# Performance work log

Measured on AMD Instinct MI355X. Metric: run time of the kernel, lower is better.

Reference implementation:

```python
import jax, jax.numpy as jnp
import numpy as np

N_NODES = 50000


def gcn_layer(x, src, dst, W, b):
    # GCNConv: out = D^{-1/2} (A + I) D^{-1/2} (x W) + b
    n = x.shape[0]
    h = x @ W  # [N, C_out]
    # degree including self-loop (count of incoming edges at dst + 1)
    deg = jnp.zeros((n,), dtype=x.dtype).at[dst].add(1.0) + 1.0
    dinv_sqrt = jax.lax.rsqrt(deg)
    norm = dinv_sqrt[src] * dinv_sqrt[dst]  # [E]
    agg = jax.ops.segment_sum(h[src] * norm[:, None], dst, num_segments=n)
    # self-loop contribution: norm_ii = 1/deg_i
    agg = agg + h * (dinv_sqrt * dinv_sqrt)[:, None]
    return agg + b


def setup_inputs() -> dict:
    key = jax.random.key(0)
    k1, k2, k3, k4, k5, k6 = jax.random.split(key, 6)
    in_c, hid_c, out_c = 128, 128, 64
    x = jax.random.normal(k1, (N_NODES, in_c), dtype=jnp.float32)
    edge_index = jax.random.randint(k2, (2, 600000), 0, N_NODES, dtype=jnp.int64)
    W1 = jax.random.normal(k3, (in_c, hid_c), dtype=jnp.float32) * (1.0 / np.sqrt(in_c))
    b1 = jnp.zeros((hid_c,), dtype=jnp.float32)
    W2 = jax.random.normal(k4, (hid_c, out_c), dtype=jnp.float32) * (1.0 / np.sqrt(hid_c))
    b2 = jnp.zeros((out_c,), dtype=jnp.float32)
    return {"x": x, "edge_index": edge_index, "W1": W1, "b1": b1, "W2": W2, "b2": b2}


def reference(x, edge_index, W1, b1, W2, b2):
    src, dst = edge_index[0], edge_index[1]
    h = gcn_layer(x, src, dst, W1, b1)
    h = jax.nn.relu(h)
    out = gcn_layer(h, src, dst, W2, b2)
    return out
```

## Files before the change

kernel.cpp:

```cpp
#include <hip/hip_runtime.h>

#define IN_C 128
#define HID_C 128
#define OUT_C 64
#define CAP 40

typedef unsigned int uint;
typedef unsigned short ushort;
typedef __attribute__((ext_vector_type(8))) short short8;
typedef __attribute__((ext_vector_type(4))) float f32x4;

__device__ __forceinline__ float bf2f(ushort u) {
    return __uint_as_float(((uint)u) << 16);
}
__device__ __forceinline__ ushort f2bf(float f) {
    uint u = __float_as_uint(f);
    return (ushort)((u + 0x7fffu + ((u >> 16) & 1u)) >> 16);
}


__global__ void prep0_kernel(int* __restrict__ cursor, int n,
                             const float* __restrict__ W1, ushort* __restrict__ w1h,
                             ushort* __restrict__ w1l, const float* __restrict__ W2,
                             ushort* __restrict__ w2h, ushort* __restrict__ w2l) {
    int idx = blockIdx.x * blockDim.x + threadIdx.x;
    if (idx < n) {
        cursor[idx] = 0;
    } else if (idx < n + 128 * 128) {
        int i1 = idx - n;
        int k = i1 >> 7, c = i1 & 127;
        float w = W1[i1];
        ushort h = f2bf(w);
        ushort l = f2bf(w - bf2f(h));
        w1h[c * 128 + k] = h;
        w1l[c * 128 + k] = l;
    } else if (idx < n + 128 * 128 + 128 * 64) {
        int i2 = idx - n - 128 * 128;
        int k = i2 >> 6, c = i2 & 63;
        float w = W2[i2];
        ushort h = f2bf(w);
        ushort l = f2bf(w - bf2f(h));
        w2h[c * 128 + k] = h;
        w2l[c * 128 + k] = l;
    }
}


#define LSTR 40

__global__ __launch_bounds__(256) void gemm1_edge_kernel(
    const float* __restrict__ A, const ushort* __restrict__ BTh,
    const ushort* __restrict__ BTl, ushort* __restrict__ C, int M, int gblocks,
    const int* __restrict__ src, const int* __restrict__ dst,
    int* __restrict__ cursor, int* __restrict__ csr_src, int E) {
    constexpr int BN = 128;
    constexpr int NT = BN / 16;
    __shared__ ushort sAh[64 * LSTR], sAl[64 * LSTR];
    __shared__ ushort sBh[BN * LSTR], sBl[BN * LSTR];

    const int tid = threadIdx.x;

    if (blockIdx.x >= gblocks) {
        int e = (blockIdx.x - gblocks) * 256 + tid;
        if (e < E) {
            unsigned s = (unsigned)src[e];
            unsigned d = (unsigned)dst[e];
            if (s < (unsigned)M && d < (unsigned)M) {
                int p = atomicAdd(&cursor[d], 1);
                if (p < CAP) csr_src[d * CAP + p] = (int)s;
            }
        }
        return;
    }

    const int w = tid >> 6;
    const int lane = tid & 63;
    const int m = lane & 15;
    const int quad = lane >> 4;
    const int r0 = blockIdx.x * 64;

    f32x4 acc[NT];
#pragma unroll
    for (int t = 0; t < NT; ++t) acc[t] = (f32x4){0.f, 0.f, 0.f, 0.f};

    for (int k0 = 0; k0 < 128; k0 += 32) {
#pragma unroll
        for (int it = 0; it < 2; ++it) {
            int idx = tid + it * 256;
            int row = idx >> 3;
            int c4 = idx & 7;
            int grow = r0 + row;
            float4 v = make_float4(0.f, 0.f, 0.f, 0.f);
            if (grow < M) v = *(const float4*)&A[(size_t)grow * 128 + k0 + c4 * 4];
            ushort h0 = f2bf(v.x), h1 = f2bf(v.y), h2 = f2bf(v.z), h3 = f2bf(v.w);
            ushort l0 = f2bf(v.x - bf2f(h0)), l1 = f2bf(v.y - bf2f(h1));
            ushort l2 = f2bf(v.z - bf2f(h2)), l3 = f2bf(v.w - bf2f(h3));
            *(ushort4*)&sAh[row * LSTR + c4 * 4] = make_ushort4(h0, h1, h2, h3);
            *(ushort4*)&sAl[row * LSTR + c4 * 4] = make_ushort4(l0, l1, l2, l3);
        }
        for (int idx = tid; idx < BN * 4; idx += 256) {
            int row = idx >> 2;
            int c = idx & 3;
            *(uint4*)&sBh[row * LSTR + c * 8] = *(const uint4*)&BTh[row * 128 + k0 + c * 8];
            *(uint4*)&sBl[row * LSTR + c * 8] = *(const uint4*)&BTl[row * 128 + k0 + c * 8];
        }
        __syncthreads();

        short8 ah = *(const short8*)&sAh[(w * 16 + m) * LSTR + quad * 8];
        short8 al = *(const short8*)&sAl[(w * 16 + m) * LSTR + quad * 8];
#pragma unroll
        for (int t = 0; t < NT; ++t) {
            short8 bh = *(const short8*)&sBh[(t * 16 + m) * LSTR + quad * 8];
            short8 bl = *(const short8*)&sBl[(t * 16 + m) * LSTR + quad * 8];
            acc[t] = __builtin_amdgcn_mfma_f32_16x16x32_bf16(ah, bh, acc[t], 0, 0, 0);
            acc[t] = __builtin_amdgcn_mfma_f32_16x16x32_bf16(al, bh, acc[t], 0, 0, 0);
            acc[t] = __builtin_amdgcn_mfma_f32_16x16x32_bf16(ah, bl, acc[t], 0, 0, 0);
        }
        __syncthreads();
    }

#pragma unroll
    for (int t = 0; t < NT; ++t) {
#pragma unroll
        for (int r = 0; r < 4; ++r) {
            int row = r0 + w * 16 + quad * 4 + r;
            if (row < M) C[(size_t)row * BN + t * 16 + m] = f2bf(acc[t][r]);
        }
    }
}


template <int BN>
__global__ __launch_bounds__(256) void gemm_mfma_bf16A(const ushort* __restrict__ A,
                                                       const ushort* __restrict__ BTh,
                                                       const ushort* __restrict__ BTl,
                                                       ushort* __restrict__ C, int M) {
    constexpr int NT = BN / 16;
    __shared__ ushort sA[64 * LSTR];
    __shared__ ushort sBh[BN * LSTR], sBl[BN * LSTR];

    const int tid = threadIdx.x;
    const int w = tid >> 6;
    const int lane = tid & 63;
    const int m = lane & 15;
    const int quad = lane >> 4;
    const int r0 = blockIdx.x * 64;

    f32x4 acc[NT];
#pragma unroll
    for (int t = 0; t < NT; ++t) acc[t] = (f32x4){0.f, 0.f, 0.f, 0.f};

    for (int k0 = 0; k0 < 128; k0 += 32) {
        {
            int row = tid >> 2;
            int c = tid & 3;
            int grow = r0 + row;
            uint4 v = make_uint4(0, 0, 0, 0);
            if (grow < M) v = *(const uint4*)&A[(size_t)grow * 128 + k0 + c * 8];
            *(uint4*)&sA[row * LSTR + c * 8] = v;
        }
        for (int idx = tid; idx < BN * 4; idx += 256) {
            int row = idx >> 2;
            int c = idx & 3;
            *(uint4*)&sBh[row * LSTR + c * 8] = *(const uint4*)&BTh[row * 128 + k0 + c * 8];
            *(uint4*)&sBl[row * LSTR + c * 8] = *(const uint4*)&BTl[row * 128 + k0 + c * 8];
        }
        __syncthreads();

        short8 ah = *(const short8*)&sA[(w * 16 + m) * LSTR + quad * 8];
#pragma unroll
        for (int t = 0; t < NT; ++t) {
            short8 bh = *(const short8*)&sBh[(t * 16 + m) * LSTR + quad * 8];
            short8 bl = *(const short8*)&sBl[(t * 16 + m) * LSTR + quad * 8];
            acc[t] = __builtin_amdgcn_mfma_f32_16x16x32_bf16(ah, bh, acc[t], 0, 0, 0);
            acc[t] = __builtin_amdgcn_mfma_f32_16x16x32_bf16(ah, bl, acc[t], 0, 0, 0);
        }
        __syncthreads();
    }

#pragma unroll
    for (int t = 0; t < NT; ++t) {
#pragma unroll
        for (int r = 0; r < 4; ++r) {
            int row = r0 + w * 16 + quad * 4 + r;
            if (row < M) C[(size_t)row * BN + t * 16 + m] = f2bf(acc[t][r]);
        }
    }
}


__global__ __launch_bounds__(256) void agg128_kernel(
    const ushort4* __restrict__ h4, const int* __restrict__ csr_src,
    const int* __restrict__ degs, const float* __restrict__ bias,
    ushort4* __restrict__ out, int n) {
    int node = blockIdx.x * 4 + (threadIdx.x >> 6);
    if (node >= n) return;
    int lane = threadIdx.x & 63;
    int half = lane >> 5;
    int q = lane & 31;
    int cnt = min(degs[node], CAP);
    float degf = (float)(cnt + 1);
    float dinv_d = rsqrtf(degf);
    int start = node * CAP;
    float a0 = 0.f, a1 = 0.f, a2 = 0.f, a3 = 0.f;

    {
        int rem = cnt;
        int es = (lane < rem) ? csr_src[start + lane] : 0;
        int cs = (lane < rem) ? degs[es] : 0;
        float en = rsqrtf((float)(cs + 1)) * dinv_d;
        int j = 0;
#define A128_PAIR(J)                                                     \
        {                                                                \
            int s0 = __shfl(es, (J)), s1 = __shfl(es, (J) + 1);          \
            float n0 = __shfl(en, (J)), n1 = __shfl(en, (J) + 1);        \
            int ss = half ? s1 : s0;                                     \
            float nn = half ? n1 : n0;                                   \
            ushort4 v = h4[(size_t)ss * 32 + q];                         \
            a0 += nn * bf2f(v.x); a1 += nn * bf2f(v.y);                  \
            a2 += nn * bf2f(v.z); a3 += nn * bf2f(v.w);                  \
        }
        for (; j + 8 <= rem; j += 8) {
            A128_PAIR(j); A128_PAIR(j + 2); A128_PAIR(j + 4); A128_PAIR(j + 6);
        }
        for (; j + 2 <= rem; j += 2) { A128_PAIR(j); }
        if (j < rem) {
            int s0 = __shfl(es, j);
            float n0 = __shfl(en, j);
            float nn = half ? 0.f : n0;
            ushort4 v = h4[(size_t)s0 * 32 + q];
            a0 += nn * bf2f(v.x); a1 += nn * bf2f(v.y);
            a2 += nn * bf2f(v.z); a3 += nn * bf2f(v.w);
        }
#undef A128_PAIR
    }

    a0 += __shfl_xor(a0, 32);
    a1 += __shfl_xor(a1, 32);
    a2 += __shfl_xor(a2, 32);
    a3 += __shfl_xor(a3, 32);
    if (half == 0) {
        ushort4 sv = h4[(size_t)node * 32 + q];
        float sn = 1.0f / degf;
        float4 bq = ((const float4*)bias)[q];
        a0 = fmaxf(a0 + bf2f(sv.x) * sn + bq.x, 0.f);
        a1 = fmaxf(a1 + bf2f(sv.y) * sn + bq.y, 0.f);
        a2 = fmaxf(a2 + bf2f(sv.z) * sn + bq.z, 0.f);
        a3 = fmaxf(a3 + bf2f(sv.w) * sn + bq.w, 0.f);
        out[(size_t)node * 32 + q] = make_ushort4(f2bf(a0), f2bf(a1), f2bf(a2), f2bf(a3));
    }
}


__global__ __launch_bounds__(256) void agg64_kernel(
    const ushort4* __restrict__ h4, const int* __restrict__ csr_src,
    const int* __restrict__ degs, const float* __restrict__ bias,
    float* __restrict__ out, int n) {
    int node = blockIdx.x * 4 + (threadIdx.x >> 6);
    if (node >= n) return;
    int lane = threadIdx.x & 63;
    int quarter = lane >> 4;
    int q = lane & 15;
    int cnt = min(degs[node], CAP);
    float degf = (float)(cnt + 1);
    float dinv_d = rsqrtf(degf);
    int start = node * CAP;
    float a0 = 0.f, a1 = 0.f, a2 = 0.f, a3 = 0.f;

    {
        int rem = cnt;
        int es = (lane < rem) ? csr_src[start + lane] : 0;
        int cs = (lane < rem) ? degs[es] : 0;
        float en = rsqrtf((float)(cs + 1)) * dinv_d;
        int j = 0;
#define A64_QUAD(J)                                                          \
        {                                                                    \
            int s0 = __shfl(es, (J)), s1 = __shfl(es, (J) + 1);              \
            int s2 = __shfl(es, (J) + 2), s3 = __shfl(es, (J) + 3);          \
            float n0 = __shfl(en, (J)), n1 = __shfl(en, (J) + 1);            \
            float n2 = __shfl(en, (J) + 2), n3 = __shfl(en, (J) + 3);        \
            int ss = (quarter & 2) ? ((quarter & 1) ? s3 : s2)               \
                                   : ((quarter & 1) ? s1 : s0);              \
            float nn = (quarter & 2) ? ((quarter & 1) ? n3 : n2)             \
                                     : ((quarter & 1) ? n1 : n0);            \
            ushort4 v = h4[(size_t)ss * 16 + q];                             \
            a0 += nn * bf2f(v.x); a1 += nn * bf2f(v.y);                      \
            a2 += nn * bf2f(v.z); a3 += nn * bf2f(v.w);                      \
        }
        for (; j + 8 <= rem; j += 8) { A64_QUAD(j); A64_QUAD(j + 4); }
        if (j + 4 <= rem) { A64_QUAD(j); j += 4; }
#undef A64_QUAD
        if (j < rem) {
            int k = j + quarter;
            int valid = (k < rem);
            int kk = valid ? k : j;
            int ss = __shfl(es, kk);
            float nv = __shfl(en, kk);
            float nn = valid ? nv : 0.f;
            ushort4 v = h4[(size_t)ss * 16 + q];
            a0 += nn * bf2f(v.x); a1 += nn * bf2f(v.y);
            a2 += nn * bf2f(v.z); a3 += nn * bf2f(v.w);
        }
    }

    a0 += __shfl_xor(a0, 16);
    a1 += __shfl_xor(a1, 16);
    a2 += __shfl_xor(a2, 16);
    a3 += __shfl_xor(a3, 16);
    a0 += __shfl_xor(a0, 32);
    a1 += __shfl_xor(a1, 32);
    a2 += __shfl_xor(a2, 32);
    a3 += __shfl_xor(a3, 32);
    if (quarter == 0) {
        ushort4 sv = h4[(size_t)node * 16 + q];
        float sn = 1.0f / degf;
        float4 bq = ((const float4*)bias)[q];
        float4 o;
        o.x = a0 + bf2f(sv.x) * sn + bq.x;
        o.y = a1 + bf2f(sv.y) * sn + bq.y;
        o.z = a2 + bf2f(sv.z) * sn + bq.z;
        o.w = a3 + bf2f(sv.w) * sn + bq.w;
        ((float4*)out)[(size_t)node * 16 + q] = o;
    }
}


extern "C" void kernel_launch(void* const* d_in, const int* in_sizes, int n_in,
                              void* d_out, int out_size, void* d_ws, size_t ws_size,
                              hipStream_t stream) {
    (void)n_in; (void)out_size; (void)ws_size;
    const float* x  = (const float*)d_in[0];
    const int*   ei = (const int*)d_in[1];
    const float* W1 = (const float*)d_in[2];
    const float* b1 = (const float*)d_in[3];
    const float* W2 = (const float*)d_in[4];
    const float* b2 = (const float*)d_in[5];
    float* out = (float*)d_out;

    const int n = in_sizes[0] / IN_C;
    const int E = in_sizes[1] / 2;
    const int* src = ei;
    const int* dst = ei + E;

    char* ws = (char*)d_ws;
    size_t off = 0;
    auto alloc = [&](size_t bytes) -> void* {
        void* p = ws + off;
        off += (bytes + 1023) & ~(size_t)1023;
        return p;
    };

    ushort* w1h     = (ushort*)alloc(128 * 128 * 2);
    ushort* w1l     = (ushort*)alloc(128 * 128 * 2);
    ushort* w2h     = (ushort*)alloc(64 * 128 * 2);
    ushort* w2l     = (ushort*)alloc(64 * 128 * 2);
    int*    cursor  = (int*)   alloc((size_t)n * 4);
    int*    csr_src = (int*)   alloc((size_t)n * CAP * 4);
    ushort* h       = (ushort*)alloc((size_t)n * HID_C * 2);
    ushort* out1b   = (ushort*)alloc((size_t)n * HID_C * 2);

    const int gblocks = (n + 63) / 64;
    const int EB = (E + 255) / 256;
    const int ablocks = (n + 3) / 4;

    prep0_kernel<<<(n + 128 * 128 + 128 * 64 + 255) / 256, 256, 0, stream>>>(
        cursor, n, W1, w1h, w1l, W2, w2h, w2l);
    gemm1_edge_kernel<<<gblocks + EB, 256, 0, stream>>>(x, w1h, w1l, h, n, gblocks,
                                                        src, dst, cursor, csr_src, E);
    agg128_kernel<<<ablocks, 256, 0, stream>>>((const ushort4*)h, csr_src, cursor,
                                               b1, (ushort4*)out1b, n);
    gemm_mfma_bf16A<OUT_C><<<gblocks, 256, 0, stream>>>(out1b, w2h, w2l, h, n);
    agg64_kernel<<<ablocks, 256, 0, stream>>>((const ushort4*)h, csr_src, cursor,
                                              b2, out, n);
}
```

Measured before the change: 178.0 us.

## Fuse layer-1 aggregation with layer-2 GEMM via shared-memory tile

Merges the 128-channel aggregation kernel and the second MFMA GEMM into one kernel. Each block aggregates 64 nodes, with each wave handling 16 nodes in sequence, and writes the ReLU'd bf16 rows into LDS. The block then multiplies that tile by W2 directly, so the intermediate activation never goes to global memory and one launch is dropped. The cost is fewer waves in the gather phase: 64 nodes per block instead of 4, plus a serial per-wave loop. That lowers memory-level parallelism for the irregular gathers, and the LDS footprint is larger.

```diff
diff --git a/kernel.cpp b/kernel.cpp
--- a/kernel.cpp
+++ b/kernel.cpp
@@ -130,36 +130,89 @@
 }
 
 
-template <int BN>
-__global__ __launch_bounds__(256) void gemm_mfma_bf16A(const ushort* __restrict__ A,
-                                                       const ushort* __restrict__ BTh,
-                                                       const ushort* __restrict__ BTl,
-                                                       ushort* __restrict__ C, int M) {
-    constexpr int NT = BN / 16;
-    __shared__ ushort sA[64 * LSTR];
-    __shared__ ushort sBh[BN * LSTR], sBl[BN * LSTR];
+#define ASTR 136
+
+__global__ __launch_bounds__(256) void agg128_gemm2_kernel(
+    const ushort4* __restrict__ h4, const int* __restrict__ csr_src,
+    const int* __restrict__ degs, const float* __restrict__ b1,
+    const ushort* __restrict__ BTh, const ushort* __restrict__ BTl,
+    ushort* __restrict__ C, int n) {
+    __shared__ ushort sA2[64 * ASTR];
+    __shared__ ushort sBh[64 * LSTR], sBl[64 * LSTR];
 
     const int tid = threadIdx.x;
     const int w = tid >> 6;
     const int lane = tid & 63;
+    const int half = lane >> 5;
+    const int q = lane & 31;
+    const int r0 = blockIdx.x * 64;
+
+    for (int i = 0; i < 16; ++i) {
+        int lrow = w * 16 + i;
+        int node = r0 + lrow;
+        float a0 = 0.f, a1 = 0.f, a2 = 0.f, a3 = 0.f;
+        if (node < n) {
+            int cnt = min(degs[node], CAP);
+            float degf = (float)(cnt + 1);
+            float dinv_d = rsqrtf(degf);
+            int start = node * CAP;
+            int rem = cnt;
+            int es = (lane < rem) ? csr_src[start + lane] : 0;
+            int cs = (lane < rem) ? degs[es] : 0;
+            float en = rsqrtf((float)(cs + 1)) * dinv_d;
+            int j = 0;
+#define A128_PAIR(J)                                                     \
+            {                                                            \
+                int s0 = __shfl(es, (J)), s1 = __shfl(es, (J) + 1);      \
+                float n0 = __shfl(en, (J)), n1 = __shfl(en, (J) + 1);    \
+                int ss = half ? s1 : s0;                                 \
+                float nn = half ? n1 : n0;                               \
+                ushort4 v = h4[(size_t)ss * 32 + q];                     \
+                a0 += nn * bf2f(v.x); a1 += nn * bf2f(v.y);              \
+                a2 += nn * bf2f(v.z); a3 += nn * bf2f(v.w);              \
+            }
+            for (; j + 8 <= rem; j += 8) {
+                A128_PAIR(j); A128_PAIR(j + 2); A128_PAIR(j + 4); A128_PAIR(j + 6);
+            }
+            for (; j + 2 <= rem; j += 2) { A128_PAIR(j); }
+            if (j < rem) {
+                int s0 = __shfl(es, j);
+                float n0 = __shfl(en, j);
+                float nn = half ? 0.f : n0;
+                ushort4 v = h4[(size_t)s0 * 32 + q];
+                a0 += nn * bf2f(v.x); a1 += nn * bf2f(v.y);
+                a2 += nn * bf2f(v.z); a3 += nn * bf2f(v.w);
+            }
+#undef A128_PAIR
+            a0 += __shfl_xor(a0, 32);
+            a1 += __shfl_xor(a1, 32);
+            a2 += __shfl_xor(a2, 32);
+            a3 += __shfl_xor(a3, 32);
+            if (half == 0) {
+                ushort4 sv = h4[(size_t)node * 32 + q];
+                float sn = 1.0f / degf;
+                float4 bq = ((const float4*)b1)[q];
+                a0 = fmaxf(a0 + bf2f(sv.x) * sn + bq.x, 0.f);
+                a1 = fmaxf(a1 + bf2f(sv.y) * sn + bq.y, 0.f);
+                a2 = fmaxf(a2 + bf2f(sv.z) * sn + bq.z, 0.f);
+                a3 = fmaxf(a3 + bf2f(sv.w) * sn + bq.w, 0.f);
+            }
+        }
+        if (half == 0) {
+            *(ushort4*)&sA2[lrow * ASTR + q * 4] =
+                make_ushort4(f2bf(a0), f2bf(a1), f2bf(a2), f2bf(a3));
+        }
+    }
+    __syncthreads();
+
     const int m = lane & 15;
     const int quad = lane >> 4;
-    const int r0 = blockIdx.x * 64;
-
-    f32x4 acc[NT];
-#pragma unroll
-    for (int t = 0; t < NT; ++t) acc[t] = (f32x4){0.f, 0.f, 0.f, 0.f};
+    f32x4 acc[4];
+#pragma unroll
+    for (int t = 0; t < 4; ++t) acc[t] = (f32x4){0.f, 0.f, 0.f, 0.f};
 
     for (int k0 = 0; k0 < 128; k0 += 32) {
-        {
-            int row = tid >> 2;
-            int c = tid & 3;
-            int grow = r0 + row;
-            uint4 v = make_uint4(0, 0, 0, 0);
-            if (grow < M) v = *(const uint4*)&A[(size_t)grow * 128 + k0 + c * 8];
-            *(uint4*)&sA[row * LSTR + c * 8] = v;
-        }
-        for (int idx = tid; idx < BN * 4; idx += 256) {
+        for (int idx = tid; idx < 64 * 4; idx += 256) {
             int row = idx >> 2;
             int c = idx & 3;
             *(uint4*)&sBh[row * LSTR + c * 8] = *(const uint4*)&BTh[row * 128 + k0 + c * 8];
@@ -167,9 +220,9 @@
         }
         __syncthreads();
 
-        short8 ah = *(const short8*)&sA[(w * 16 + m) * LSTR + quad * 8];
-#pragma unroll
-        for (int t = 0; t < NT; ++t) {
+        short8 ah = *(const short8*)&sA2[(w * 16 + m) * ASTR + k0 + quad * 8];
+#pragma unroll
+        for (int t = 0; t < 4; ++t) {
             short8 bh = *(const short8*)&sBh[(t * 16 + m) * LSTR + quad * 8];
             short8 bl = *(const short8*)&sBl[(t * 16 + m) * LSTR + quad * 8];
             acc[t] = __builtin_amdgcn_mfma_f32_16x16x32_bf16(ah, bh, acc[t], 0, 0, 0);
@@ -179,75 +232,12 @@
     }
 
 #pragma unroll
-    for (int t = 0; t < NT; ++t) {
+    for (int t = 0; t < 4; ++t) {
 #pragma unroll
         for (int r = 0; r < 4; ++r) {
             int row = r0 + w * 16 + quad * 4 + r;
-            if (row < M) C[(size_t)row * BN + t * 16 + m] = f2bf(acc[t][r]);
-        }
-    }
-}
-
-
-__global__ __launch_bounds__(256) void agg128_kernel(
-    const ushort4* __restrict__ h4, const int* __restrict__ csr_src,
-    const int* __restrict__ degs, const float* __restrict__ bias,
-    ushort4* __restrict__ out, int n) {
-    int node = blockIdx.x * 4 + (threadIdx.x >> 6);
-    if (node >= n) return;
-    int lane = threadIdx.x & 63;
-    int half = lane >> 5;
-    int q = lane & 31;
-    int cnt = min(degs[node], CAP);
-    float degf = (float)(cnt + 1);
-    float dinv_d = rsqrtf(degf);
-    int start = node * CAP;
-    float a0 = 0.f, a1 = 0.f, a2 = 0.f, a3 = 0.f;
-
-    {
-        int rem = cnt;
-        int es = (lane < rem) ? csr_src[start + lane] : 0;
-        int cs = (lane < rem) ? degs[es] : 0;
-        float en = rsqrtf((float)(cs + 1)) * dinv_d;
-        int j = 0;
-#define A128_PAIR(J)                                                     \
-        {                                                                \
-            int s0 = __shfl(es, (J)), s1 = __shfl(es, (J) + 1);          \
-            float n0 = __shfl(en, (J)), n1 = __shfl(en, (J) + 1);        \
-            int ss = half ? s1 : s0;                                     \
-            float nn = half ? n1 : n0;                                   \
-            ushort4 v = h4[(size_t)ss * 32 + q];                         \
-            a0 += nn * bf2f(v.x); a1 += nn * bf2f(v.y);                  \
-            a2 += nn * bf2f(v.z); a3 += nn * bf2f(v.w);                  \
-        }
-        for (; j + 8 <= rem; j += 8) {
-            A128_PAIR(j); A128_PAIR(j + 2); A128_PAIR(j + 4); A128_PAIR(j + 6);
-        }
-        for (; j + 2 <= rem; j += 2) { A128_PAIR(j); }
-        if (j < rem) {
-            int s0 = __shfl(es, j);
-            float n0 = __shfl(en, j);
-            float nn = half ? 0.f : n0;
-            ushort4 v = h4[(size_t)s0 * 32 + q];
-            a0 += nn * bf2f(v.x); a1 += nn * bf2f(v.y);
-            a2 += nn * bf2f(v.z); a3 += nn * bf2f(v.w);
-        }
-#undef A128_PAIR
-    }
-
-    a0 += __shfl_xor(a0, 32);
-    a1 += __shfl_xor(a1, 32);
-    a2 += __shfl_xor(a2, 32);
-    a3 += __shfl_xor(a3, 32);
-    if (half == 0) {
-        ushort4 sv = h4[(size_t)node * 32 + q];
-        float sn = 1.0f / degf;
-        float4 bq = ((const float4*)bias)[q];
-        a0 = fmaxf(a0 + bf2f(sv.x) * sn + bq.x, 0.f);
-        a1 = fmaxf(a1 + bf2f(sv.y) * sn + bq.y, 0.f);
-        a2 = fmaxf(a2 + bf2f(sv.z) * sn + bq.z, 0.f);
-        a3 = fmaxf(a3 + bf2f(sv.w) * sn + bq.w, 0.f);
-        out[(size_t)node * 32 + q] = make_ushort4(f2bf(a0), f2bf(a1), f2bf(a2), f2bf(a3));
+            if (row < n) C[(size_t)row * 64 + t * 16 + m] = f2bf(acc[t][r]);
+        }
     }
 }
 
@@ -357,7 +347,7 @@
     int*    cursor  = (int*)   alloc((size_t)n * 4);
     int*    csr_src = (int*)   alloc((size_t)n * CAP * 4);
     ushort* h       = (ushort*)alloc((size_t)n * HID_C * 2);
-    ushort* out1b   = (ushort*)alloc((size_t)n * HID_C * 2);
+    ushort* h2      = (ushort*)alloc((size_t)n * OUT_C * 2);
 
     const int gblocks = (n + 63) / 64;
     const int EB = (E + 255) / 256;
@@ -367,9 +357,8 @@
         cursor, n, W1, w1h, w1l, W2, w2h, w2l);
     gemm1_edge_kernel<<<gblocks + EB, 256, 0, stream>>>(x, w1h, w1l, h, n, gblocks,
                                                         src, dst, cursor, csr_src, E);
-    agg128_kernel<<<ablocks, 256, 0, stream>>>((const ushort4*)h, csr_src, cursor,
-                                               b1, (ushort4*)out1b, n);
-    gemm_mfma_bf16A<OUT_C><<<gblocks, 256, 0, stream>>>(out1b, w2h, w2l, h, n);
-    agg64_kernel<<<ablocks, 256, 0, stream>>>((const ushort4*)h, csr_src, cursor,
+    agg128_gemm2_kernel<<<gblocks, 256, 0, stream>>>((const ushort4*)h, csr_src, cursor,
+                                                     b1, w2h, w2l, h2, n);
+    agg64_kernel<<<ablocks, 256, 0, stream>>>((const ushort4*)h2, csr_src, cursor,
                                               b2, out, n);
 }
```

Result: slower. 191.4 us (+7.5%).
